# Performance work log

Measured on AMD Instinct MI355X. Metric: run time of the kernel, lower is better.

The kernel has to match this reference:

```python
import jax, jax.numpy as jnp
import numpy as np
from jax import lax

EPS = 1e-7  # keras backend epsilon used by K.ctc_batch_cost
NEG = -1e30  # log-space 'zero'


def setup_inputs() -> dict:
    key = jax.random.key(0)
    k1, k2 = jax.random.split(key)
    B, T, C, L = 512, 512, 128, 48
    # softmax-like probabilities over classes (ctc_batch_cost expects probs)
    u = jax.random.uniform(k1, (B, T, C), dtype=jnp.float32, minval=1e-3, maxval=1.0)
    y_pred = u / jnp.sum(u, axis=-1, keepdims=True)
    # labels in [0, C-2]; blank index is C-1 (keras convention)
    y_true = jax.random.randint(k2, (B, L), 0, C - 1, dtype=jnp.int64)
    return {"y_true": y_true, "y_pred": y_pred}


def _ctc_loss(y_true, y_pred):
    # y_true: [B, L] int labels; y_pred: [B, T, C] probabilities
    B, T, C = y_pred.shape
    L = y_true.shape[1]
    S = 2 * L + 1
    blank = C - 1

    log_probs = jnp.log(y_pred + EPS)  # [B, T, C]

    # extended label sequence: blank, l1, blank, l2, ..., blank -> [B, S]
    ext = jnp.full((B, S), blank, dtype=y_true.dtype).at[:, 1::2].set(y_true)
    ext_m2 = jnp.concatenate(
        [jnp.full((B, 2), -1, dtype=ext.dtype), ext[:, :-2]], axis=1
    )
    # skip-transition allowed iff current symbol is a non-blank differing from s-2
    skip = (ext != blank) & (ext != ext_m2)  # [B, S]

    # gather per-extended-symbol log probs: [B, T, S] -> time-major [T, B, S]
    lp_ext = jnp.take_along_axis(log_probs, ext[:, None, :], axis=2)
    lp_ext = jnp.moveaxis(lp_ext, 1, 0)

    neg = jnp.asarray(NEG, log_probs.dtype)
    alpha0 = jnp.full((B, S), neg)
    alpha0 = alpha0.at[:, 0].set(lp_ext[0, :, 0]).at[:, 1].set(lp_ext[0, :, 1])

    def step(alpha, lp_t):
        a1 = alpha
        a2 = jnp.concatenate([jnp.full((B, 1), neg), alpha[:, :-1]], axis=1)
        a3 = jnp.concatenate([jnp.full((B, 2), neg), alpha[:, :-2]], axis=1)
        a3 = jnp.where(skip, a3, neg)
        new = jnp.logaddexp(jnp.logaddexp(a1, a2), a3) + lp_t
        return new, None

    alpha_T, _ = lax.scan(step, alpha0, lp_ext[1:])
    # total log-likelihood ends in last blank or last label
    loglik = jnp.logaddexp(alpha_T[:, -1], alpha_T[:, -2])
    return -loglik[:, None]  # [B, 1] like K.ctc_batch_cost


def reference(y_true, y_pred):
    return _ctc_loss(y_true, y_pred)
```

## Files before the change

### kernel.cpp

```cpp
#include <hip/hip_runtime.h>


constexpr int Bc = 512, Tc = 512, Cc = 128, Lc = 48;
constexpr float FEPS = 1e-7f;
constexpr float FNEG = -1e30f;
constexpr float LN2F = 0.69314718055994530942f;
constexpr int CDEAD = -(1 << 28);

#define DPP_WAVE_SHR1 0x138
#define DPP_WAVE_SHL1 0x130

__device__ __forceinline__ float dppf_shr1(float x) {
    return __int_as_float(__builtin_amdgcn_update_dpp(
        0, __float_as_int(x), DPP_WAVE_SHR1, 0xF, 0xF, false));
}
__device__ __forceinline__ float dppf_shl1(float x) {
    return __int_as_float(__builtin_amdgcn_update_dpp(
        0, __float_as_int(x), DPP_WAVE_SHL1, 0xF, 0xF, false));
}
__device__ __forceinline__ int dppi_shr1_self(int c) {
    return __builtin_amdgcn_update_dpp(c, c, DPP_WAVE_SHR1, 0xF, 0xF, false);
}
__device__ __forceinline__ int dppi_shl1_self(int c) {
    return __builtin_amdgcn_update_dpp(c, c, DPP_WAVE_SHL1, 0xF, 0xF, false);
}

__device__ __forceinline__ float lae2(float a, float b) {
    float m = fmaxf(a, b);
    float d = fabsf(a - b);
    return m + __log2f(1.0f + __builtin_amdgcn_exp2f(-d));
}
__device__ __forceinline__ float blankp(float praw) {
    return __uint_as_float((unsigned)
        __builtin_amdgcn_readlane(__float_as_uint(praw), 63)) + FEPS;
}

__global__ __launch_bounds__(128)
void ctc_fb_kernel(const int* __restrict__ y_true,
                   const float* __restrict__ y_pred,
                   float* __restrict__ out) {
    const int b = blockIdx.x;
    const int lane = threadIdx.x & 63;
    const int wave = threadIdx.x >> 6;

    const float* yb = y_pred + (size_t)b * Tc * Cc;

    const int lab = (lane < Lc) ? y_true[b * Lc + lane] : (Cc - 1);
    const int labm1 = __builtin_amdgcn_ds_bpermute(((lane + 63) & 63) << 2, lab);
    const int labp1 = __builtin_amdgcn_ds_bpermute(((lane + 1) & 63) << 2, lab);
    const bool skip  = (lab != (Cc - 1)) && (lab != labm1);
    const bool skipN = (labp1 != (Cc - 1)) && (labp1 != lab);
    const bool validhi = (lane < Lc);
    const bool lane0 = (lane == 0);

    __shared__ float sblo[64], sbhi[64];
    __shared__ int sbc[64];

    float lo = 0.0f, hi = 0.0f;
    int c = CDEAD;

    auto renorm = [&]() {
        float mx = fmaxf(lo, hi);
        int e = (int)((__float_as_uint(mx) >> 23) & 0xFF) - 127;
        e = (mx > 0.0f) ? e : 0;
        lo = ldexpf(lo, -e);
        hi = ldexpf(hi, -e);
        c += e;
    };

    if (wave == 0) {
        auto dostep = [&](float praw) {
            float pb = blankp(praw);
            float ph = validhi ? (praw + FEPS) : 0.0f;
            float sh  = dppf_shr1(hi);
            int   cm1 = dppi_shr1_self(c);
            bool  own_dead = (lo == 0.0f) && (hi == 0.0f);
            int   m  = own_dead ? cm1 : ((c > cm1) ? c : cm1);
            float lov = ldexpf(lo, c - m);
            float hiv = ldexpf(hi, c - m);
            float shv = ldexpf(sh, cm1 - m);
            float a3  = skip ? shv : 0.0f;
            lo = (lov + shv) * pb;
            hi = (hiv + lov + a3) * ph;
            c = m;
        };
        float pf[32];
        #pragma unroll
        for (int j = 0; j < 32; ++j) pf[j] = yb[j * Cc + lab];
        {
            float praw = pf[0];
            pf[0] = yb[32 * Cc + lab];
            float pb0 = blankp(praw);
            lo = lane0 ? pb0 : 0.0f;
            hi = lane0 ? (praw + FEPS) : 0.0f;
            c  = lane0 ? 0 : CDEAD;
            #pragma unroll
            for (int j = 1; j < 32; ++j) {
                float r = pf[j];
                pf[j] = yb[(32 + j) * Cc + lab];
                dostep(r);
                if ((j & 7) == 7) renorm();
            }
        }
        #pragma unroll 1
        for (int g = 1; g < 7; ++g) {
            const float* ybg = yb + (size_t)(g * 32 + 32) * Cc;
            #pragma unroll
            for (int j = 0; j < 32; ++j) {
                float r = pf[j];
                pf[j] = ybg[j * Cc + lab];
                dostep(r);
                if ((j & 7) == 7) renorm();
            }
        }
        #pragma unroll
        for (int j = 0; j < 32; ++j) {
            dostep(pf[j]);
            if ((j & 7) == 7) renorm();
        }
    } else {
        auto dostep = [&](float praw) {
            float pb = blankp(praw);
            float ph = validhi ? (praw + FEPS) : 0.0f;
            float qlo = lo * pb;
            float qhi = hi * ph;
            float qlo_n = dppf_shl1(qlo);
            float qhi_n = dppf_shl1(qhi);
            int   cp1 = dppi_shl1_self(c);
            bool  own_dead = (qlo == 0.0f) && (qhi == 0.0f);
            int   m  = own_dead ? cp1 : ((c > cp1) ? c : cp1);
            float nb = skipN ? (qlo_n + qhi_n) : qlo_n;
            lo = ldexpf(qlo + qhi, c - m);
            hi = ldexpf(qhi, c - m) + ldexpf(nb, cp1 - m);
            c = m;
        };
        lo = (lane == 48) ? 1.0f : 0.0f;
        hi = (lane == 47) ? 1.0f : 0.0f;
        c = (lane == 47 || lane == 48) ? 0 : CDEAD;
        float pf[32];
        #pragma unroll
        for (int j = 0; j < 32; ++j) pf[j] = yb[(size_t)(511 - j) * Cc + lab];
        #pragma unroll 1
        for (int g = 0; g < 7; ++g) {
            #pragma unroll
            for (int j = 0; j < 32; ++j) {
                float r = pf[j];
                pf[j] = yb[(size_t)(511 - (g * 32 + 32 + j)) * Cc + lab];
                dostep(r);
                if ((j & 7) == 7) renorm();
            }
        }
        #pragma unroll
        for (int j = 0; j < 32; ++j) {
            dostep(pf[j]);
            if ((j & 7) == 7) renorm();
        }
        sblo[lane] = lo;
        sbhi[lane] = hi;
        sbc[lane]  = c;
    }

    __syncthreads();

    if (wave == 0) {
        float blo = sblo[lane], bhi = sbhi[lane];
        float ctot = (float)(c + sbc[lane]);
        float plo = lo * blo;
        float phi = hi * bhi;
        float yl = (plo > 0.0f) ? (__log2f(plo) + ctot) : FNEG;
        float yh = (phi > 0.0f) ? (__log2f(phi) + ctot) : FNEG;
        float v = lae2(yl, yh);
        #pragma unroll
        for (int mk = 1; mk < 64; mk <<= 1)
            v = lae2(v, __shfl_xor(v, mk, 64));
        if (lane0) out[b] = -(v * LN2F);
    }
}

extern "C" void kernel_launch(void* const* d_in, const int* in_sizes, int n_in,
                              void* d_out, int out_size, void* d_ws, size_t ws_size,
                              hipStream_t stream) {
    const int* y_true = (const int*)d_in[0];
    const float* y_pred = (const float*)d_in[1];
    float* out = (float*)d_out;
    hipLaunchKernelGGL(ctc_fb_kernel, dim3(Bc), dim3(128), 0, stream,
                       y_true, y_pred, out);
}
```

Baseline: 31.88 us.

## Batch blank-prob readlanes per 16-step chunk and simplify backward skip shift

The prefetch pipeline now works on 16-step chunks instead of 32. Each chunk's blank probabilities (readlane 63) and label probabilities are precomputed into arrays before the dependent recurrence runs. This moves the scalar readlane and epsilon adds off the serial alpha/beta critical path. The backward step folds the skip condition into the sending lane, so it does one DPP shift instead of two and no longer needs the labp1 bpermute. The cost is a shallower prefetch window and more register arrays, which may expose more load latency.

```diff
diff --git a/kernel.cpp b/kernel.cpp
--- a/kernel.cpp
+++ b/kernel.cpp
@@ -30,9 +30,9 @@
     float d = fabsf(a - b);
     return m + __log2f(1.0f + __builtin_amdgcn_exp2f(-d));
 }
-__device__ __forceinline__ float blankp(float praw) {
+__device__ __forceinline__ float rd63f(float v) {
     return __uint_as_float((unsigned)
-        __builtin_amdgcn_readlane(__float_as_uint(praw), 63)) + FEPS;
+        __builtin_amdgcn_readlane(__float_as_uint(v), 63));
 }
 
 __global__ __launch_bounds__(128)
@@ -47,9 +47,7 @@
 
     const int lab = (lane < Lc) ? y_true[b * Lc + lane] : (Cc - 1);
     const int labm1 = __builtin_amdgcn_ds_bpermute(((lane + 63) & 63) << 2, lab);
-    const int labp1 = __builtin_amdgcn_ds_bpermute(((lane + 1) & 63) << 2, lab);
     const bool skip  = (lab != (Cc - 1)) && (lab != labm1);
-    const bool skipN = (labp1 != (Cc - 1)) && (labp1 != lab);
     const bool validhi = (lane < Lc);
     const bool lane0 = (lane == 0);
 
@@ -68,10 +66,17 @@
         c += e;
     };
 
+    float praw[16], pbf[16], phf[16];
+    auto batch = [&]() {
+        #pragma unroll
+        for (int j = 0; j < 16; ++j) {
+            pbf[j] = rd63f(praw[j]) + FEPS;
+            phf[j] = validhi ? (praw[j] + FEPS) : 0.0f;
+        }
+    };
+
     if (wave == 0) {
-        auto dostep = [&](float praw) {
-            float pb = blankp(praw);
-            float ph = validhi ? (praw + FEPS) : 0.0f;
+        auto step = [&](int j) {
             float sh  = dppf_shr1(hi);
             int   cm1 = dppi_shr1_self(c);
             bool  own_dead = (lo == 0.0f) && (hi == 0.0f);
@@ -80,80 +85,72 @@
             float hiv = ldexpf(hi, c - m);
             float shv = ldexpf(sh, cm1 - m);
             float a3  = skip ? shv : 0.0f;
-            lo = (lov + shv) * pb;
-            hi = (hiv + lov + a3) * ph;
+            lo = (lov + shv) * pbf[j];
+            hi = (hiv + lov + a3) * phf[j];
             c = m;
         };
-        float pf[32];
         #pragma unroll
-        for (int j = 0; j < 32; ++j) pf[j] = yb[j * Cc + lab];
+        for (int j = 0; j < 16; ++j) praw[j] = yb[j * Cc + lab];
         {
-            float praw = pf[0];
-            pf[0] = yb[32 * Cc + lab];
-            float pb0 = blankp(praw);
-            lo = lane0 ? pb0 : 0.0f;
-            hi = lane0 ? (praw + FEPS) : 0.0f;
+            batch();
+            const float* ybn = yb + (size_t)16 * Cc + lab;
+            #pragma unroll
+            for (int j = 0; j < 16; ++j) praw[j] = ybn[(size_t)j * Cc];
+            lo = lane0 ? pbf[0] : 0.0f;
+            hi = lane0 ? phf[0] : 0.0f;
             c  = lane0 ? 0 : CDEAD;
             #pragma unroll
-            for (int j = 1; j < 32; ++j) {
-                float r = pf[j];
-                pf[j] = yb[(32 + j) * Cc + lab];
-                dostep(r);
-                if ((j & 7) == 7) renorm();
+            for (int j = 1; j < 16; ++j) {
+                step(j);
+                if (j == 7 || j == 15) renorm();
             }
         }
         #pragma unroll 1
-        for (int g = 1; g < 7; ++g) {
-            const float* ybg = yb + (size_t)(g * 32 + 32) * Cc;
+        for (int g = 1; g < 16; ++g) {
+            batch();
+            if (g < 15) {
+                const float* ybn = yb + (size_t)((g + 1) * 16) * Cc + lab;
+                #pragma unroll
+                for (int j = 0; j < 16; ++j) praw[j] = ybn[(size_t)j * Cc];
+            }
             #pragma unroll
-            for (int j = 0; j < 32; ++j) {
-                float r = pf[j];
-                pf[j] = ybg[j * Cc + lab];
-                dostep(r);
-                if ((j & 7) == 7) renorm();
+            for (int j = 0; j < 16; ++j) {
+                step(j);
+                if (j == 7 || j == 15) renorm();
             }
         }
-        #pragma unroll
-        for (int j = 0; j < 32; ++j) {
-            dostep(pf[j]);
-            if ((j & 7) == 7) renorm();
-        }
     } else {
-        auto dostep = [&](float praw) {
-            float pb = blankp(praw);
-            float ph = validhi ? (praw + FEPS) : 0.0f;
-            float qlo = lo * pb;
-            float qhi = hi * ph;
-            float qlo_n = dppf_shl1(qlo);
-            float qhi_n = dppf_shl1(qhi);
+        auto step = [&](int j) {
+            float qlo = lo * pbf[j];
+            float qhi = hi * phf[j];
+            float u   = qlo + (skip ? qhi : 0.0f);
+            float un  = dppf_shl1(u);
             int   cp1 = dppi_shl1_self(c);
             bool  own_dead = (qlo == 0.0f) && (qhi == 0.0f);
             int   m  = own_dead ? cp1 : ((c > cp1) ? c : cp1);
-            float nb = skipN ? (qlo_n + qhi_n) : qlo_n;
             lo = ldexpf(qlo + qhi, c - m);
-            hi = ldexpf(qhi, c - m) + ldexpf(nb, cp1 - m);
+            hi = ldexpf(qhi, c - m) + ldexpf(un, cp1 - m);
             c = m;
         };
         lo = (lane == 48) ? 1.0f : 0.0f;
         hi = (lane == 47) ? 1.0f : 0.0f;
-        c = (lane == 47 || lane == 48) ? 0 : CDEAD;
-        float pf[32];
+        c  = (lane == 47 || lane == 48) ? 0 : CDEAD;
         #pragma unroll
-        for (int j = 0; j < 32; ++j) pf[j] = yb[(size_t)(511 - j) * Cc + lab];
+        for (int j = 0; j < 16; ++j) praw[j] = yb[(size_t)(511 - j) * Cc + lab];
         #pragma unroll 1
-        for (int g = 0; g < 7; ++g) {
+        for (int g = 0; g < 16; ++g) {
+            batch();
+            if (g < 15) {
+                const float* ybn = yb + lab;
+                const int t0 = 511 - (g + 1) * 16;
+                #pragma unroll
+                for (int j = 0; j < 16; ++j) praw[j] = ybn[(size_t)(t0 - j) * Cc];
+            }
             #pragma unroll
-            for (int j = 0; j < 32; ++j) {
-                float r = pf[j];
-                pf[j] = yb[(size_t)(511 - (g * 32 + 32 + j)) * Cc + lab];
-                dostep(r);
-                if ((j & 7) == 7) renorm();
+            for (int j = 0; j < 16; ++j) {
+                step(j);
+                if (j == 7 || j == 15) renorm();
             }
-        }
-        #pragma unroll
-        for (int j = 0; j < 32; ++j) {
-            dostep(pf[j]);
-            if ((j & 7) == 7) renorm();
         }
         sblo[lane] = lo;
         sbhi[lane] = hi;
```

Result: faster. 29.82 us (-6.5%).
